# Optimization experiments

Measured on AMD Instinct MI355X. Metric: run time of the kernel, lower is better.

## Reference

```python
import jax, jax.numpy as jnp
import numpy as np

H = 16   # num_attention_heads
HD = 12  # head_dim = 192 / 16
W = 2    # one-sided window = attention_window // 2
EPS = 1e-12  # HF layer_norm_eps default
NEG = jnp.finfo(jnp.float32).min


def _shift(a, d):
    """out[:, i] = a[:, i + d], zero-padded out of range (shift along axis 1)."""
    if d == 0:
        return a
    S = a.shape[1]
    pad = [(0, 0)] * a.ndim
    if d > 0:
        pad[1] = (0, d)
        return jnp.pad(a, pad)[:, d:d + S]
    pad[1] = (-d, 0)
    return jnp.pad(a, pad)[:, :S]


def setup_inputs() -> dict:
    key = jax.random.key(0)
    ks = jax.random.split(key, 6)
    B, S, D = 16, 8192, 192
    sc = 1.0 / np.sqrt(D)
    return {
        "x": jax.random.normal(ks[0], (B, S, D), jnp.float32),
        "mask0": jnp.zeros((B, S), jnp.float32),
        "Wq": jax.random.normal(ks[1], (D, D), jnp.float32) * sc,
        "bq": jnp.zeros((D,), jnp.float32),
        "Wk": jax.random.normal(ks[2], (D, D), jnp.float32) * sc,
        "bk": jnp.zeros((D,), jnp.float32),
        "Wv": jax.random.normal(ks[3], (D, D), jnp.float32) * sc,
        "bv": jnp.zeros((D,), jnp.float32),
        "Wo": jax.random.normal(ks[4], (D, D), jnp.float32) * sc,
        "bo": jnp.zeros((D,), jnp.float32),
        "ln_g": jnp.ones((D,), jnp.float32),
        "ln_b": jnp.zeros((D,), jnp.float32),
    }


def reference(x, mask0, Wq, bq, Wk, bk, Wv, bv, Wo, bo, ln_g, ln_b):
    B, S, D = x.shape
    # projections; query pre-scaled by sqrt(head_dim) as in HF Longformer
    q = (x @ Wq.T + bq).reshape(B, S, H, HD) / jnp.sqrt(jnp.float32(HD))
    k = (x @ Wk.T + bk).reshape(B, S, H, HD)
    v = (x @ Wv.T + bv).reshape(B, S, H, HD)

    # additive key-side mask (finfo.min where attention_mask != 0)
    float_mask = jnp.where(mask0 != 0, NEG, jnp.float32(0.0))  # (B, S)
    idx = jnp.arange(S)

    # banded scores: scores[b, i, h, d+W] = q[b,i,h] . k[b,i+d,h]
    band = []
    for d in range(-W, W + 1):
        s = jnp.einsum('bshd,bshd->bsh', q, _shift(k, d))
        s = s + _shift(float_mask, d)[:, :, None]
        valid = (idx + d >= 0) & (idx + d < S)  # (S,)
        s = jnp.where(valid[None, :, None], s, -jnp.inf)
        band.append(s)
    scores = jnp.stack(band, axis=-1)  # (B, S, H, 2W+1)

    probs = jax.nn.softmax(scores, axis=-1)
    is_index_masked = mask0 < 0
    probs = jnp.where(is_index_masked[:, :, None, None], jnp.float32(0.0), probs)

    # banded PV: ctx[b,i,h] = sum_d probs[b,i,h,d+W] * v[b,i+d,h]
    ctx = jnp.zeros_like(v)
    for i, d in enumerate(range(-W, W + 1)):
        ctx = ctx + probs[..., i:i + 1] * _shift(v, d)
    attn = ctx.reshape(B, S, D)

    # LongformerSelfOutput: dense -> residual -> LayerNorm (dropout=eval identity)
    h = attn @ Wo.T + bo + x
    mu = jnp.mean(h, axis=-1, keepdims=True)
    var = jnp.mean((h - mu) ** 2, axis=-1, keepdims=True)
    return (h - mu) / jnp.sqrt(var + EPS) * ln_g + ln_b
```

## Files before the change

kernel.cpp:

```cpp
#include <hip/hip_runtime.h>
#include <stdint.h>

#define SEQ 8192
#define BATCH 16
#define DM 192
#define NROWS (BATCH*SEQ)

#define WS_NEED 294912u
#define WO_OFF_U 110592

typedef __attribute__((ext_vector_type(8))) short bf16x8;
typedef __attribute__((ext_vector_type(4))) float f32x4;

static __device__ __forceinline__ ushort f2bf(float f){
  uint u = __float_as_uint(f);
  u += 0x7fffu + ((u >> 16) & 1u);
  return (ushort)(u >> 16);
}
static __device__ __forceinline__ bf16x8 cvt8(const float* p){
  float4 lo = *(const float4*)p;
  float4 hi = *(const float4*)(p + 4);
  bf16x8 t;
  t[0] = (short)f2bf(lo.x); t[1] = (short)f2bf(lo.y);
  t[2] = (short)f2bf(lo.z); t[3] = (short)f2bf(lo.w);
  t[4] = (short)f2bf(hi.x); t[5] = (short)f2bf(hi.y);
  t[6] = (short)f2bf(hi.z); t[7] = (short)f2bf(hi.w);
  return t;
}
static __device__ __forceinline__ void unpack2(uint u, float& lo, float& hi){
  lo = __uint_as_float(u << 16);
  hi = __uint_as_float(u & 0xffff0000u);
}

__global__ void pack_w(const float* __restrict__ Wq, const float* __restrict__ Wk,
                       const float* __restrict__ Wv, const float* __restrict__ Wo,
                       ushort* __restrict__ wp)
{
  const int f = blockIdx.x;
  const int lane = threadIdx.x;
  const int lm = lane & 15, quad = lane >> 4;
  const float* src;
  size_t dst;
  int kt;
  if (f < 216) {
    kt = f % 6; int t = f / 6; int nt = t % 9; int w = t / 9;
    int n = w * 144 + nt * 16 + lm;
    int proj = n / DM, cin = n - proj * DM;
    src = ((proj == 0) ? Wq : (proj == 1) ? Wk : Wv) + (size_t)cin * DM;
    dst = (size_t)f * 512 + (size_t)lane * 8;
  } else {
    int fo = f - 216;
    kt = fo % 6; int t = fo / 6; int nt = t % 3; int w = t / 3;
    int n = w * 48 + nt * 16 + lm;
    src = Wo + (size_t)n * DM;
    dst = (size_t)WO_OFF_U + (size_t)fo * 512 + (size_t)lane * 8;
  }
  const int k0 = kt * 32 + quad * 8;
  *(bf16x8*)(wp + dst) = cvt8(src + k0);
}

template<int PK>
__global__ __launch_bounds__(256) void qkv_attn_t(
    const float* __restrict__ x,
    const float* __restrict__ Wq, const float* __restrict__ bq,
    const float* __restrict__ Wk, const float* __restrict__ bk,
    const float* __restrict__ Wv, const float* __restrict__ bv,
    const float* __restrict__ mask0,
    float* ctxo, const ushort* __restrict__ wp)
{
  __shared__ ushort ks[68][192];
  __shared__ ushort vs[68][192];
  __shared__ ushort xs[68][72];
  __shared__ float  ms[68];

  const int tid  = threadIdx.x;
  const int wave = tid >> 6, lane = tid & 63;
  const int lm   = lane & 15, quad = lane >> 4;
  const int m0   = blockIdx.x * 64;
  const int wbase = wave * 144;

  if (tid < 68) {
    int g = min(max(m0 - 2 + tid, 0), NROWS - 1);
    ms[tid] = mask0[g];
  }

  const float* wrow[9];
  float bias9[9];
  int proj9[9], cin9[9];
  #pragma unroll
  for (int nt = 0; nt < 9; nt++) {
    const int n = wbase + nt * 16 + lm;
    const int proj = n / DM;
    const int cin  = n - proj * DM;
    proj9[nt] = proj; cin9[nt] = cin;
    bias9[nt] = (proj == 0) ? bq[cin] : (proj == 1) ? bk[cin] : bv[cin];
    if constexpr (!PK) {
      const float* w = (proj == 0) ? Wq : (proj == 1) ? Wk : Wv;
      wrow[nt] = w + (size_t)cin * DM;
    }
  }

  f32x4 acc[5][9];
  #pragma unroll
  for (int a = 0; a < 5; a++)
    #pragma unroll
    for (int b = 0; b < 9; b++) acc[a][b] = (f32x4){0.f, 0.f, 0.f, 0.f};

  for (int st = 0; st < 3; st++) {
    __syncthreads();
    for (int ch = tid; ch < 1088; ch += 256) {
      const int r = ch >> 4, c4 = (ch & 15) << 2;
      const int g = min(max(m0 - 2 + r, 0), NROWS - 1);
      float4 f = *(const float4*)(x + (size_t)g * DM + st * 64 + c4);
      ushort4 u;
      u.x = f2bf(f.x); u.y = f2bf(f.y); u.z = f2bf(f.z); u.w = f2bf(f.w);
      *(ushort4*)&xs[r][c4] = u;
    }
    __syncthreads();
    #pragma unroll
    for (int half = 0; half < 2; half++) {
      const int kt = st * 2 + half;
      const int k0 = kt * 32 + quad * 8;
      const int kl = half * 32 + quad * 8;
      bf16x8 af[5];
      #pragma unroll
      for (int mt = 0; mt < 5; mt++) {
        int lrow = mt * 16 + lm;
        lrow = min(lrow, 67);
        af[mt] = *(const bf16x8*)&xs[lrow][kl];
      }
      #pragma unroll
      for (int nt = 0; nt < 9; nt++) {
        bf16x8 bfm;
        if constexpr (PK)
          bfm = *(const bf16x8*)(wp + ((size_t)((wave * 9 + nt) * 6 + kt)) * 512
                                    + (size_t)lane * 8);
        else
          bfm = cvt8(wrow[nt] + k0);
        #pragma unroll
        for (int mt = 0; mt < 5; mt++)
          acc[mt][nt] = __builtin_amdgcn_mfma_f32_16x16x32_bf16(af[mt], bfm, acc[mt][nt], 0, 0, 0);
      }
    }
  }

  const float qscale = 0.28867513459481287f;
  #pragma unroll
  for (int nt = 0; nt < 9; nt++) {
    const int proj = proj9[nt], cin = cin9[nt];
    const float bsv = bias9[nt];
    #pragma unroll
    for (int mt = 0; mt < 5; mt++) {
      #pragma unroll
      for (int r = 0; r < 4; r++) {
        int lrow = mt * 16 + quad * 4 + r;
        float vv = acc[mt][nt][r] + bsv;
        if (proj == 0) {
          if (lrow >= 2 && lrow < 66)
            ctxo[(size_t)(m0 + lrow - 2) * DM + cin] = vv * qscale;
        } else if (proj == 1) {
          if (lrow < 68) ks[lrow][cin] = f2bf(vv);
        } else {
          if (lrow < 68) vs[lrow][cin] = f2bf(vv);
        }
      }
    }
  }
  __syncthreads();

  const float NEGF = -3.402823466e38f;
  #pragma unroll
  for (int it = 0; it < 4; it++) {
    const int pair = it * 256 + tid;
    const int h = pair & 15, lr = pair >> 4;
    const int row = m0 + lr;
    const int s = row & 8191;

    float* qp = ctxo + (size_t)row * DM + h * 12;
    float4 q0 = *(const float4*)(qp);
    float4 q1 = *(const float4*)(qp + 4);
    float4 q2 = *(const float4*)(qp + 8);
    float qf[12] = {q0.x, q0.y, q0.z, q0.w, q1.x, q1.y, q1.z, q1.w,
                    q2.x, q2.y, q2.z, q2.w};

    float sc[5];
    #pragma unroll
    for (int d = 0; d < 5; d++) {
      int j = s + d - 2;
      if (j < 0 || j >= SEQ) { sc[d] = -INFINITY; continue; }
      float kf[12];
      const uint2* p = (const uint2*)&ks[lr + d][h * 12];
      uint2 t0 = p[0], t1 = p[1], t2 = p[2];
      unpack2(t0.x, kf[0], kf[1]);  unpack2(t0.y, kf[2], kf[3]);
      unpack2(t1.x, kf[4], kf[5]);  unpack2(t1.y, kf[6], kf[7]);
      unpack2(t2.x, kf[8], kf[9]);  unpack2(t2.y, kf[10], kf[11]);
      float dot = 0.f;
      #pragma unroll
      for (int t = 0; t < 12; t++) dot += qf[t] * kf[t];
      float fm = (ms[lr + d] != 0.0f) ? NEGF : 0.0f;
      sc[d] = dot + fm;
    }

    float mx = sc[0];
    #pragma unroll
    for (int d = 1; d < 5; d++) mx = fmaxf(mx, sc[d]);
    float e[5], sum = 0.f;
    #pragma unroll
    for (int d = 0; d < 5; d++) { e[d] = __expf(sc[d] - mx); sum += e[d]; }
    float inv = 1.0f / sum;
    const bool zrow = (ms[lr + 2] < 0.0f);

    float cf[12];
    #pragma unroll
    for (int t = 0; t < 12; t++) cf[t] = 0.f;
    #pragma unroll
    for (int d = 0; d < 5; d++) {
      float p = zrow ? 0.f : e[d] * inv;
      float vf[12];
      const uint2* pv = (const uint2*)&vs[lr + d][h * 12];
      uint2 t0 = pv[0], t1 = pv[1], t2 = pv[2];
      unpack2(t0.x, vf[0], vf[1]);  unpack2(t0.y, vf[2], vf[3]);
      unpack2(t1.x, vf[4], vf[5]);  unpack2(t1.y, vf[6], vf[7]);
      unpack2(t2.x, vf[8], vf[9]);  unpack2(t2.y, vf[10], vf[11]);
      #pragma unroll
      for (int t = 0; t < 12; t++) cf[t] += p * vf[t];
    }

    *(float4*)(qp + 0) = make_float4(cf[0], cf[1], cf[2], cf[3]);
    *(float4*)(qp + 4) = make_float4(cf[4], cf[5], cf[6], cf[7]);
    *(float4*)(qp + 8) = make_float4(cf[8], cf[9], cf[10], cf[11]);
  }
}

template<int PK>
__global__ __launch_bounds__(256) void out_ln_t(
    const float* attn, const float* __restrict__ Wo,
    const float* __restrict__ bo, const float* __restrict__ x,
    const float* __restrict__ g, const float* __restrict__ beta,
    float* out, const ushort* __restrict__ wp)
{
  __shared__ float hs[64][200];
  __shared__ float red[64][8];
  __shared__ float stats[64][2];

  const int tid  = threadIdx.x;
  const int wave = tid >> 6, lane = tid & 63;
  const int lm   = lane & 15, quad = lane >> 4;
  const int m0   = blockIdx.x * 64;
  const int wbase = wave * 48;

  f32x4 acc[4][3];
  #pragma unroll
  for (int a = 0; a < 4; a++)
    #pragma unroll
    for (int b = 0; b < 3; b++) acc[a][b] = (f32x4){0.f, 0.f, 0.f, 0.f};

  for (int kt = 0; kt < 6; kt++) {
    const int k0 = kt * 32 + quad * 8;
    bf16x8 af[4];
    #pragma unroll
    for (int mt = 0; mt < 4; mt++)
      af[mt] = cvt8(attn + (size_t)(m0 + mt * 16 + lm) * DM + k0);
    #pragma unroll
    for (int nt = 0; nt < 3; nt++) {
      bf16x8 bfm;
      if constexpr (PK)
        bfm = *(const bf16x8*)(wp + WO_OFF_U
                                  + ((size_t)((wave * 3 + nt) * 6 + kt)) * 512
                                  + (size_t)lane * 8);
      else {
        const int n = wbase + nt * 16 + lm;
        bfm = cvt8(Wo + (size_t)n * DM + k0);
      }
      #pragma unroll
      for (int mt = 0; mt < 4; mt++)
        acc[mt][nt] = __builtin_amdgcn_mfma_f32_16x16x32_bf16(af[mt], bfm, acc[mt][nt], 0, 0, 0);
    }
  }

  #pragma unroll
  for (int nt = 0; nt < 3; nt++) {
    const int n = wbase + nt * 16 + lm;
    const float bsv = bo[n];
    #pragma unroll
    for (int mt = 0; mt < 4; mt++) {
      #pragma unroll
      for (int r = 0; r < 4; r++) {
        int rl = mt * 16 + quad * 4 + r;
        hs[rl][n] = acc[mt][nt][r] + bsv + x[(size_t)(m0 + rl) * DM + n];
      }
    }
  }
  __syncthreads();

  {
    int row = tid >> 2, seg = tid & 3;
    float s = 0.f, s2 = 0.f;
    #pragma unroll
    for (int c = 0; c < 48; c++) {
      float t = hs[row][seg * 48 + c];
      s += t; s2 += t * t;
    }
    red[row][seg] = s;
    red[row][4 + seg] = s2;
  }
  __syncthreads();
  if (tid < 64) {
    float sum = red[tid][0] + red[tid][1] + red[tid][2] + red[tid][3];
    float sq  = red[tid][4] + red[tid][5] + red[tid][6] + red[tid][7];
    float mu  = sum * (1.f / 192.f);
    float var = sq * (1.f / 192.f) - mu * mu;
    stats[tid][0] = mu;
    stats[tid][1] = rsqrtf(var + 1e-12f);
  }
  __syncthreads();

  #pragma unroll
  for (int it = 0; it < 12; it++) {
    int idx = tid + it * 256;
    int row = idx / 48, c4 = idx - row * 48;
    float4 hv = *(const float4*)&hs[row][c4 * 4];
    float mu = stats[row][0], rs = stats[row][1];
    float4 gg = *(const float4*)(g + c4 * 4);
    float4 bb = *(const float4*)(beta + c4 * 4);
    float4 o;
    o.x = (hv.x - mu) * rs * gg.x + bb.x;
    o.y = (hv.y - mu) * rs * gg.y + bb.y;
    o.z = (hv.z - mu) * rs * gg.z + bb.z;
    o.w = (hv.w - mu) * rs * gg.w + bb.w;
    *(float4*)(out + (size_t)(m0 + row) * DM + c4 * 4) = o;
  }
}

extern "C" void kernel_launch(void* const* d_in, const int* in_sizes, int n_in,
                              void* d_out, int out_size, void* d_ws, size_t ws_size,
                              hipStream_t stream)
{
  const float* x    = (const float*)d_in[0];
  const float* mask0= (const float*)d_in[1];
  const float* Wq   = (const float*)d_in[2];
  const float* bq   = (const float*)d_in[3];
  const float* Wk   = (const float*)d_in[4];
  const float* bk   = (const float*)d_in[5];
  const float* Wv   = (const float*)d_in[6];
  const float* bv   = (const float*)d_in[7];
  const float* Wo   = (const float*)d_in[8];
  const float* bo   = (const float*)d_in[9];
  const float* lng  = (const float*)d_in[10];
  const float* lnb  = (const float*)d_in[11];
  float* out = (float*)d_out;

  if (d_ws != nullptr && ws_size >= (size_t)WS_NEED) {
    ushort* wp = (ushort*)d_ws;
    pack_w<<<288, 64, 0, stream>>>(Wq, Wk, Wv, Wo, wp);
    qkv_attn_t<1><<<NROWS / 64, 256, 0, stream>>>(x, Wq, bq, Wk, bk, Wv, bv, mask0, out, wp);
    out_ln_t<1><<<NROWS / 64, 256, 0, stream>>>(out, Wo, bo, x, lng, lnb, out, wp);
  } else {
    qkv_attn_t<0><<<NROWS / 64, 256, 0, stream>>>(x, Wq, bq, Wk, bk, Wv, bv, mask0, out, nullptr);
    out_ln_t<0><<<NROWS / 64, 256, 0, stream>>>(out, Wo, bo, x, lng, lnb, out, nullptr);
  }
}
```

Measured before the change: 507.4 us.

## Fuse QKV-attention and output-projection LayerNorm into one kernel

Merges the QKV projection plus banded attention kernel with the output-projection, residual and LayerNorm kernel into a single kernel. The bf16 context stays in LDS, reusing the K/V buffer, so the fp32 context no longer makes a round trip to global memory. LayerNorm statistics are now reduced with in-register shuffles instead of a shared-memory row buffer. The cost is a larger combined LDS footprint and more register pressure per block, which may lower occupancy; Q is still written to the output buffer as scratch. The fallback path without a workspace is reworked separately to stage the attention tile and residual in LDS.

```diff
diff --git a/kernel.cpp b/kernel.cpp
--- a/kernel.cpp
+++ b/kernel.cpp
@@ -8,6 +8,15 @@
 
 #define WS_NEED 294912u
 #define WO_OFF_U 110592
+
+#define OFF_KS   0
+#define OFF_VS   26112
+#define OFF_XS   52224
+#define OFF_MS   62016
+#define OFF_RS   62288
+#define OFF_RQ   63312
+#define OFF_ST   64336
+#define LDS_TOTAL 64848
 
 typedef __attribute__((ext_vector_type(8))) short bf16x8;
 typedef __attribute__((ext_vector_type(4))) float f32x4;
@@ -59,19 +68,25 @@
   *(bf16x8*)(wp + dst) = cvt8(src + k0);
 }
 
-template<int PK>
-__global__ __launch_bounds__(256) void qkv_attn_t(
+__global__ __launch_bounds__(256) void fused_t(
     const float* __restrict__ x,
     const float* __restrict__ Wq, const float* __restrict__ bq,
     const float* __restrict__ Wk, const float* __restrict__ bk,
     const float* __restrict__ Wv, const float* __restrict__ bv,
     const float* __restrict__ mask0,
-    float* ctxo, const ushort* __restrict__ wp)
+    const float* __restrict__ Wo, const float* __restrict__ bo,
+    const float* __restrict__ g, const float* __restrict__ beta,
+    float* out, const ushort* __restrict__ wp)
 {
-  __shared__ ushort ks[68][192];
-  __shared__ ushort vs[68][192];
-  __shared__ ushort xs[68][72];
-  __shared__ float  ms[68];
+  __shared__ __align__(16) char smem[LDS_TOTAL];
+  ushort (*ks)[192] = (ushort(*)[192])(smem + OFF_KS);
+  ushort (*vs)[192] = (ushort(*)[192])(smem + OFF_VS);
+  ushort (*xs)[72]  = (ushort(*)[72]) (smem + OFF_XS);
+  ushort* ctxL      = (ushort*)(smem + OFF_KS);
+  float*  ms        = (float*) (smem + OFF_MS);
+  float*  red_s     = (float*) (smem + OFF_RS);
+  float*  red_q     = (float*) (smem + OFF_RQ);
+  float*  stats     = (float*) (smem + OFF_ST);
 
   const int tid  = threadIdx.x;
   const int wave = tid >> 6, lane = tid & 63;
@@ -80,11 +95,10 @@
   const int wbase = wave * 144;
 
   if (tid < 68) {
-    int g = min(max(m0 - 2 + tid, 0), NROWS - 1);
-    ms[tid] = mask0[g];
-  }
-
-  const float* wrow[9];
+    int gr = min(max(m0 - 2 + tid, 0), NROWS - 1);
+    ms[tid] = mask0[gr];
+  }
+
   float bias9[9];
   int proj9[9], cin9[9];
   #pragma unroll
@@ -94,10 +108,6 @@
     const int cin  = n - proj * DM;
     proj9[nt] = proj; cin9[nt] = cin;
     bias9[nt] = (proj == 0) ? bq[cin] : (proj == 1) ? bk[cin] : bv[cin];
-    if constexpr (!PK) {
-      const float* w = (proj == 0) ? Wq : (proj == 1) ? Wk : Wv;
-      wrow[nt] = w + (size_t)cin * DM;
-    }
   }
 
   f32x4 acc[5][9];
@@ -110,8 +120,266 @@
     __syncthreads();
     for (int ch = tid; ch < 1088; ch += 256) {
       const int r = ch >> 4, c4 = (ch & 15) << 2;
-      const int g = min(max(m0 - 2 + r, 0), NROWS - 1);
-      float4 f = *(const float4*)(x + (size_t)g * DM + st * 64 + c4);
+      const int gr = min(max(m0 - 2 + r, 0), NROWS - 1);
+      float4 f = *(const float4*)(x + (size_t)gr * DM + st * 64 + c4);
+      ushort4 u;
+      u.x = f2bf(f.x); u.y = f2bf(f.y); u.z = f2bf(f.z); u.w = f2bf(f.w);
+      *(ushort4*)&xs[r][c4] = u;
+    }
+    __syncthreads();
+    #pragma unroll
+    for (int half = 0; half < 2; half++) {
+      const int kt = st * 2 + half;
+      const int kl = half * 32 + quad * 8;
+      bf16x8 af[5];
+      #pragma unroll
+      for (int mt = 0; mt < 5; mt++) {
+        int lrow = mt * 16 + lm;
+        lrow = min(lrow, 67);
+        af[mt] = *(const bf16x8*)&xs[lrow][kl];
+      }
+      #pragma unroll
+      for (int nt = 0; nt < 9; nt++) {
+        bf16x8 bfm = *(const bf16x8*)(wp + ((size_t)((wave * 9 + nt) * 6 + kt)) * 512
+                                         + (size_t)lane * 8);
+        #pragma unroll
+        for (int mt = 0; mt < 5; mt++)
+          acc[mt][nt] = __builtin_amdgcn_mfma_f32_16x16x32_bf16(af[mt], bfm, acc[mt][nt], 0, 0, 0);
+      }
+    }
+  }
+
+  const float qscale = 0.28867513459481287f;
+  #pragma unroll
+  for (int nt = 0; nt < 9; nt++) {
+    const int proj = proj9[nt], cin = cin9[nt];
+    const float bsv = bias9[nt];
+    #pragma unroll
+    for (int mt = 0; mt < 5; mt++) {
+      #pragma unroll
+      for (int r = 0; r < 4; r++) {
+        int lrow = mt * 16 + quad * 4 + r;
+        float vv = acc[mt][nt][r] + bsv;
+        if (proj == 0) {
+          if (lrow >= 2 && lrow < 66)
+            out[(size_t)(m0 + lrow - 2) * DM + cin] = vv * qscale;
+        } else if (proj == 1) {
+          if (lrow < 68) ks[lrow][cin] = f2bf(vv);
+        } else {
+          if (lrow < 68) vs[lrow][cin] = f2bf(vv);
+        }
+      }
+    }
+  }
+  __syncthreads();
+
+  const float NEGF = -3.402823466e38f;
+  float cfa[4][12];
+  #pragma unroll
+  for (int it = 0; it < 4; it++) {
+    const int pair = it * 256 + tid;
+    const int h = pair & 15, lr = pair >> 4;
+    const int row = m0 + lr;
+    const int s = row & 8191;
+
+    const float* qp = out + (size_t)row * DM + h * 12;
+    float4 q0 = *(const float4*)(qp);
+    float4 q1 = *(const float4*)(qp + 4);
+    float4 q2 = *(const float4*)(qp + 8);
+    float qf[12] = {q0.x, q0.y, q0.z, q0.w, q1.x, q1.y, q1.z, q1.w,
+                    q2.x, q2.y, q2.z, q2.w};
+
+    float sc[5];
+    #pragma unroll
+    for (int d = 0; d < 5; d++) {
+      int j = s + d - 2;
+      if (j < 0 || j >= SEQ) { sc[d] = -INFINITY; continue; }
+      float kf[12];
+      const uint2* p = (const uint2*)&ks[lr + d][h * 12];
+      uint2 t0 = p[0], t1 = p[1], t2 = p[2];
+      unpack2(t0.x, kf[0], kf[1]);  unpack2(t0.y, kf[2], kf[3]);
+      unpack2(t1.x, kf[4], kf[5]);  unpack2(t1.y, kf[6], kf[7]);
+      unpack2(t2.x, kf[8], kf[9]);  unpack2(t2.y, kf[10], kf[11]);
+      float dot = 0.f;
+      #pragma unroll
+      for (int t = 0; t < 12; t++) dot += qf[t] * kf[t];
+      float fm = (ms[lr + d] != 0.0f) ? NEGF : 0.0f;
+      sc[d] = dot + fm;
+    }
+
+    float mx = sc[0];
+    #pragma unroll
+    for (int d = 1; d < 5; d++) mx = fmaxf(mx, sc[d]);
+    float e[5], sum = 0.f;
+    #pragma unroll
+    for (int d = 0; d < 5; d++) { e[d] = __expf(sc[d] - mx); sum += e[d]; }
+    float inv = 1.0f / sum;
+    const bool zrow = (ms[lr + 2] < 0.0f);
+
+    #pragma unroll
+    for (int t = 0; t < 12; t++) cfa[it][t] = 0.f;
+    #pragma unroll
+    for (int d = 0; d < 5; d++) {
+      float p = zrow ? 0.f : e[d] * inv;
+      float vf[12];
+      const uint2* pv = (const uint2*)&vs[lr + d][h * 12];
+      uint2 t0 = pv[0], t1 = pv[1], t2 = pv[2];
+      unpack2(t0.x, vf[0], vf[1]);  unpack2(t0.y, vf[2], vf[3]);
+      unpack2(t1.x, vf[4], vf[5]);  unpack2(t1.y, vf[6], vf[7]);
+      unpack2(t2.x, vf[8], vf[9]);  unpack2(t2.y, vf[10], vf[11]);
+      #pragma unroll
+      for (int t = 0; t < 12; t++) cfa[it][t] += p * vf[t];
+    }
+  }
+  __syncthreads();
+
+  #pragma unroll
+  for (int it = 0; it < 4; it++) {
+    const int pair = it * 256 + tid;
+    const int h = pair & 15, lr = pair >> 4;
+    ushort* cp = ctxL + lr * 208 + h * 12;
+    #pragma unroll
+    for (int t = 0; t < 6; t++) {
+      uint u = (uint)f2bf(cfa[it][2*t]) | ((uint)f2bf(cfa[it][2*t+1]) << 16);
+      *(uint*)(cp + 2*t) = u;
+    }
+  }
+  __syncthreads();
+
+  const int wbase2 = wave * 48;
+  f32x4 acc2[4][3];
+  #pragma unroll
+  for (int a = 0; a < 4; a++)
+    #pragma unroll
+    for (int b = 0; b < 3; b++) acc2[a][b] = (f32x4){0.f, 0.f, 0.f, 0.f};
+
+  #pragma unroll
+  for (int kt = 0; kt < 6; kt++) {
+    const int k0 = kt * 32 + quad * 8;
+    bf16x8 af[4];
+    #pragma unroll
+    for (int mt = 0; mt < 4; mt++)
+      af[mt] = *(const bf16x8*)(ctxL + (mt * 16 + lm) * 208 + k0);
+    #pragma unroll
+    for (int nt = 0; nt < 3; nt++) {
+      bf16x8 bfm = *(const bf16x8*)(wp + WO_OFF_U
+                                       + ((size_t)((wave * 3 + nt) * 6 + kt)) * 512
+                                       + (size_t)lane * 8);
+      #pragma unroll
+      for (int mt = 0; mt < 4; mt++)
+        acc2[mt][nt] = __builtin_amdgcn_mfma_f32_16x16x32_bf16(af[mt], bfm, acc2[mt][nt], 0, 0, 0);
+    }
+  }
+
+  float bo3[3], gv[3], bv2[3];
+  #pragma unroll
+  for (int nt = 0; nt < 3; nt++) {
+    int n = wbase2 + nt * 16 + lm;
+    bo3[nt] = bo[n]; gv[nt] = g[n]; bv2[nt] = beta[n];
+  }
+  #pragma unroll
+  for (int nt = 0; nt < 3; nt++) {
+    int n = wbase2 + nt * 16 + lm;
+    #pragma unroll
+    for (int mt = 0; mt < 4; mt++)
+      #pragma unroll
+      for (int r = 0; r < 4; r++) {
+        int rl = mt * 16 + quad * 4 + r;
+        acc2[mt][nt][r] += bo3[nt] + x[(size_t)(m0 + rl) * DM + n];
+      }
+  }
+  #pragma unroll
+  for (int mt = 0; mt < 4; mt++)
+    #pragma unroll
+    for (int r = 0; r < 4; r++) {
+      float s  = acc2[mt][0][r] + acc2[mt][1][r] + acc2[mt][2][r];
+      float q2 = acc2[mt][0][r]*acc2[mt][0][r] + acc2[mt][1][r]*acc2[mt][1][r]
+               + acc2[mt][2][r]*acc2[mt][2][r];
+      #pragma unroll
+      for (int off = 1; off < 16; off <<= 1) {
+        s  += __shfl_xor(s,  off, 64);
+        q2 += __shfl_xor(q2, off, 64);
+      }
+      if (lm == 0) {
+        int rl = mt * 16 + quad * 4 + r;
+        red_s[rl * 4 + wave] = s;
+        red_q[rl * 4 + wave] = q2;
+      }
+    }
+  __syncthreads();
+  if (tid < 64) {
+    float sum = red_s[tid*4] + red_s[tid*4+1] + red_s[tid*4+2] + red_s[tid*4+3];
+    float sq  = red_q[tid*4] + red_q[tid*4+1] + red_q[tid*4+2] + red_q[tid*4+3];
+    float mu  = sum * (1.f / 192.f);
+    float var = sq * (1.f / 192.f) - mu * mu;
+    stats[tid*2]   = mu;
+    stats[tid*2+1] = rsqrtf(var + 1e-12f);
+  }
+  __syncthreads();
+  #pragma unroll
+  for (int mt = 0; mt < 4; mt++)
+    #pragma unroll
+    for (int r = 0; r < 4; r++) {
+      int rl = mt * 16 + quad * 4 + r;
+      float mu = stats[rl*2], rs = stats[rl*2+1];
+      #pragma unroll
+      for (int nt = 0; nt < 3; nt++) {
+        int n = wbase2 + nt * 16 + lm;
+        out[(size_t)(m0 + rl) * DM + n] = (acc2[mt][nt][r] - mu) * rs * gv[nt] + bv2[nt];
+      }
+    }
+}
+
+__global__ __launch_bounds__(256) void qkv_attn_f(
+    const float* __restrict__ x,
+    const float* __restrict__ Wq, const float* __restrict__ bq,
+    const float* __restrict__ Wk, const float* __restrict__ bk,
+    const float* __restrict__ Wv, const float* __restrict__ bv,
+    const float* __restrict__ mask0,
+    float* ctxo)
+{
+  __shared__ ushort ks[68][192];
+  __shared__ ushort vs[68][192];
+  __shared__ ushort xs[68][72];
+  __shared__ float  ms[68];
+
+  const int tid  = threadIdx.x;
+  const int wave = tid >> 6, lane = tid & 63;
+  const int lm   = lane & 15, quad = lane >> 4;
+  const int m0   = blockIdx.x * 64;
+  const int wbase = wave * 144;
+
+  if (tid < 68) {
+    int gr = min(max(m0 - 2 + tid, 0), NROWS - 1);
+    ms[tid] = mask0[gr];
+  }
+
+  const float* wrow[9];
+  float bias9[9];
+  int proj9[9], cin9[9];
+  #pragma unroll
+  for (int nt = 0; nt < 9; nt++) {
+    const int n = wbase + nt * 16 + lm;
+    const int proj = n / DM;
+    const int cin  = n - proj * DM;
+    proj9[nt] = proj; cin9[nt] = cin;
+    bias9[nt] = (proj == 0) ? bq[cin] : (proj == 1) ? bk[cin] : bv[cin];
+    const float* w = (proj == 0) ? Wq : (proj == 1) ? Wk : Wv;
+    wrow[nt] = w + (size_t)cin * DM;
+  }
+
+  f32x4 acc[5][9];
+  #pragma unroll
+  for (int a = 0; a < 5; a++)
+    #pragma unroll
+    for (int b = 0; b < 9; b++) acc[a][b] = (f32x4){0.f, 0.f, 0.f, 0.f};
+
+  for (int st = 0; st < 3; st++) {
+    __syncthreads();
+    for (int ch = tid; ch < 1088; ch += 256) {
+      const int r = ch >> 4, c4 = (ch & 15) << 2;
+      const int gr = min(max(m0 - 2 + r, 0), NROWS - 1);
+      float4 f = *(const float4*)(x + (size_t)gr * DM + st * 64 + c4);
       ushort4 u;
       u.x = f2bf(f.x); u.y = f2bf(f.y); u.z = f2bf(f.z); u.w = f2bf(f.w);
       *(ushort4*)&xs[r][c4] = u;
@@ -131,12 +399,7 @@
       }
       #pragma unroll
       for (int nt = 0; nt < 9; nt++) {
-        bf16x8 bfm;
-        if constexpr (PK)
-          bfm = *(const bf16x8*)(wp + ((size_t)((wave * 9 + nt) * 6 + kt)) * 512
-                                    + (size_t)lane * 8);
-        else
-          bfm = cvt8(wrow[nt] + k0);
+        bf16x8 bfm = cvt8(wrow[nt] + k0);
         #pragma unroll
         for (int mt = 0; mt < 5; mt++)
           acc[mt][nt] = __builtin_amdgcn_mfma_f32_16x16x32_bf16(af[mt], bfm, acc[mt][nt], 0, 0, 0);
@@ -232,16 +495,16 @@
   }
 }
 
-template<int PK>
-__global__ __launch_bounds__(256) void out_ln_t(
+__global__ __launch_bounds__(256) void out_ln_f(
     const float* attn, const float* __restrict__ Wo,
     const float* __restrict__ bo, const float* __restrict__ x,
     const float* __restrict__ g, const float* __restrict__ beta,
-    float* out, const ushort* __restrict__ wp)
+    float* out)
 {
   __shared__ float hs[64][200];
   __shared__ float red[64][8];
   __shared__ float stats[64][2];
+  __shared__ ushort as_[64][72];
 
   const int tid  = threadIdx.x;
   const int wave = tid >> 6, lane = tid & 63;
@@ -249,32 +512,46 @@
   const int m0   = blockIdx.x * 64;
   const int wbase = wave * 48;
 
+  #pragma unroll
+  for (int it = 0; it < 12; it++) {
+    int idx = tid + it * 256;
+    int row = idx / 48, c4 = idx - row * 48;
+    *(float4*)&hs[row][c4 * 4] = *(const float4*)(x + (size_t)(m0 + row) * DM + c4 * 4);
+  }
+
   f32x4 acc[4][3];
   #pragma unroll
   for (int a = 0; a < 4; a++)
     #pragma unroll
     for (int b = 0; b < 3; b++) acc[a][b] = (f32x4){0.f, 0.f, 0.f, 0.f};
 
-  for (int kt = 0; kt < 6; kt++) {
-    const int k0 = kt * 32 + quad * 8;
-    bf16x8 af[4];
-    #pragma unroll
-    for (int mt = 0; mt < 4; mt++)
-      af[mt] = cvt8(attn + (size_t)(m0 + mt * 16 + lm) * DM + k0);
-    #pragma unroll
-    for (int nt = 0; nt < 3; nt++) {
-      bf16x8 bfm;
-      if constexpr (PK)
-        bfm = *(const bf16x8*)(wp + WO_OFF_U
-                                  + ((size_t)((wave * 3 + nt) * 6 + kt)) * 512
-                                  + (size_t)lane * 8);
-      else {
+  for (int st = 0; st < 3; st++) {
+    __syncthreads();
+    for (int ch = tid; ch < 1024; ch += 256) {
+      const int r = ch >> 4, c4 = (ch & 15) << 2;
+      float4 f = *(const float4*)(attn + (size_t)(m0 + r) * DM + st * 64 + c4);
+      ushort4 u;
+      u.x = f2bf(f.x); u.y = f2bf(f.y); u.z = f2bf(f.z); u.w = f2bf(f.w);
+      *(ushort4*)&as_[r][c4] = u;
+    }
+    __syncthreads();
+    #pragma unroll
+    for (int half = 0; half < 2; half++) {
+      const int kt = st * 2 + half;
+      const int k0 = kt * 32 + quad * 8;
+      const int kl = half * 32 + quad * 8;
+      bf16x8 af[4];
+      #pragma unroll
+      for (int mt = 0; mt < 4; mt++)
+        af[mt] = *(const bf16x8*)&as_[mt * 16 + lm][kl];
+      #pragma unroll
+      for (int nt = 0; nt < 3; nt++) {
         const int n = wbase + nt * 16 + lm;
-        bfm = cvt8(Wo + (size_t)n * DM + k0);
-      }
-      #pragma unroll
-      for (int mt = 0; mt < 4; mt++)
-        acc[mt][nt] = __builtin_amdgcn_mfma_f32_16x16x32_bf16(af[mt], bfm, acc[mt][nt], 0, 0, 0);
+        bf16x8 bfm = cvt8(Wo + (size_t)n * DM + k0);
+        #pragma unroll
+        for (int mt = 0; mt < 4; mt++)
+          acc[mt][nt] = __builtin_amdgcn_mfma_f32_16x16x32_bf16(af[mt], bfm, acc[mt][nt], 0, 0, 0);
+      }
     }
   }
 
@@ -287,7 +564,7 @@
       #pragma unroll
       for (int r = 0; r < 4; r++) {
         int rl = mt * 16 + quad * 4 + r;
-        hs[rl][n] = acc[mt][nt][r] + bsv + x[(size_t)(m0 + rl) * DM + n];
+        hs[rl][n] = acc[mt][nt][r] + bsv + hs[rl][n];
       }
     }
   }
@@ -353,10 +630,10 @@
   if (d_ws != nullptr && ws_size >= (size_t)WS_NEED) {
     ushort* wp = (ushort*)d_ws;
     pack_w<<<288, 64, 0, stream>>>(Wq, Wk, Wv, Wo, wp);
-    qkv_attn_t<1><<<NROWS / 64, 256, 0, stream>>>(x, Wq, bq, Wk, bk, Wv, bv, mask0, out, wp);
-    out_ln_t<1><<<NROWS / 64, 256, 0, stream>>>(out, Wo, bo, x, lng, lnb, out, wp);
+    fused_t<<<NROWS / 64, 256, 0, stream>>>(
+        x, Wq, bq, Wk, bk, Wv, bv, mask0, Wo, bo, lng, lnb, out, wp);
   } else {
-    qkv_attn_t<0><<<NROWS / 64, 256, 0, stream>>>(x, Wq, bq, Wk, bk, Wv, bv, mask0, out, nullptr);
-    out_ln_t<0><<<NROWS / 64, 256, 0, stream>>>(out, Wo, bo, x, lng, lnb, out, nullptr);
-  }
-}
+    qkv_attn_f<<<NROWS / 64, 256, 0, stream>>>(x, Wq, bq, Wk, bk, Wv, bv, mask0, out);
+    out_ln_f<<<NROWS / 64, 256, 0, stream>>>(out, Wo, bo, x, lng, lnb, out);
+  }
+}
```

Result: no change. 508.2 us (+0.2%).
